# Performance work log

Hardware: AMD Instinct MI355X
Metric: run time of the kernel (lower is better)

The kernel has to match this reference:

```python
import jax, jax.numpy as jnp
import numpy as np

B, NFIELD = 8192, 20
NFEAT = 100000
SQL_VOCAB = NFIELD + NFEAT + 1  # 100021
SQL_NEMB, DATA_NEMB = 16, 64
HID = 1024
OUT = 1
K = 16
ALPHA = 1.5
N_BISECT = 50


def entmax_bisect(x, alpha=ALPHA, n_iter=N_BISECT):
    # alpha-entmax via bisection on the threshold tau (Peters et al. 2019).
    am1 = alpha - 1.0
    x = x * am1
    d = x.shape[-1]
    max_val = jnp.max(x, axis=-1, keepdims=True)
    tau_lo = max_val - 1.0
    tau_hi = max_val - d ** (1.0 - alpha)

    def p(tau):
        return jnp.clip(x - tau, 0.0) ** (1.0 / am1)

    f_lo = jnp.sum(p(tau_lo), axis=-1, keepdims=True) - 1.0

    def body(carry, _):
        tau_lo, tau_hi, f_lo = carry
        tau_m = 0.5 * (tau_lo + tau_hi)
        f_m = jnp.sum(p(tau_m), axis=-1, keepdims=True) - 1.0
        same_side = (f_m * f_lo) >= 0
        tau_lo = jnp.where(same_side, tau_m, tau_lo)
        tau_hi = jnp.where(same_side, tau_hi, tau_m)
        f_lo = jnp.where(same_side, f_m, f_lo)
        return (tau_lo, tau_hi, f_lo), None

    (tau_lo, tau_hi, _), _ = jax.lax.scan(body, (tau_lo, tau_hi, f_lo), None, length=n_iter)
    pm = p(0.5 * (tau_lo + tau_hi))
    return pm / jnp.sum(pm, axis=-1, keepdims=True)


def cv_squared(v):
    eps = 1e-10
    var = jnp.var(v, ddof=1)  # torch .var() is unbiased
    mean = jnp.mean(v)
    return var / (mean * mean + eps)


def setup_inputs() -> dict:
    key = jax.random.key(0)
    ks = jax.random.split(key, 12)
    xavier = lambda k, shp: jax.random.uniform(k, shp, jnp.float32, -1.0, 1.0) * jnp.sqrt(6.0 / (shp[-2] + shp[-1]))
    inp = {
        "x": jax.random.randint(ks[0], (B, NFIELD), 0, NFEAT),
        "sql": jax.random.randint(ks[1], (B, NFIELD), 0, SQL_VOCAB),
        "sql_emb_table": xavier(ks[2], (SQL_VOCAB, SQL_NEMB)),
        "input_emb_table": xavier(ks[3], (NFEAT, DATA_NEMB)),
        # gate: Linear(gate_in, HID) -> ReLU -> Linear(HID, K)
        "gW1": xavier(ks[4], (NFIELD * SQL_NEMB, HID)),
        "gb1": jnp.zeros((HID,), jnp.float32),
        "gW2": xavier(ks[5], (HID, K)),
        "gb2": jnp.zeros((K,), jnp.float32),
        # K experts: Linear(in, HID) -> ReLU -> Linear(HID, OUT), stacked on axis 0
        "eW1": xavier(ks[6], (K, NFIELD * DATA_NEMB, HID)),
        "eb1": jnp.zeros((K, HID), jnp.float32),
        "eW2": xavier(ks[7], (K, HID, OUT)),
        "eb2": jnp.zeros((K, OUT), jnp.float32),
    }
    return inp


def reference(x, sql, sql_emb_table, input_emb_table, gW1, gb1, gW2, gb2, eW1, eb1, eW2, eb2):
    Bn = x.shape[0]
    x_emb = input_emb_table[x].reshape(Bn, -1)      # [B, nfield*data_nemb]
    sql_emb = sql_emb_table[sql].reshape(Bn, -1)    # [B, nfield*sql_nemb]

    # gate network + entmax-bisect (dropout is identity in eval)
    g = jax.nn.relu(sql_emb @ gW1 + gb1) @ gW2 + gb2  # [B, K]
    gate_score = entmax_bisect(g)                     # [B, K], sparse simplex

    loss = cv_squared(jnp.sum(gate_score, axis=0))

    # all K experts on every token, vectorized
    h = jax.nn.relu(jnp.einsum("bi,kih->bkh", x_emb, eW1) + eb1)  # [B, K, HID]
    y_k = jnp.einsum("bkh,kho->bko", h, eW2) + eb2                # [B, K, OUT]
    y = jnp.sum(gate_score[:, :, None] * y_k, axis=1)             # [B, OUT]
    return (y.squeeze(-1), loss)
```

## Files before the change

### kernel.cpp

```cpp
#include <hip/hip_runtime.h>
#include <stdint.h>

#define NFIELD 20
#define HID 1024
#define KEXP 16
#define KX 1280
#define KS 320
#define BATCH 8192

typedef __bf16 bf16x8 __attribute__((ext_vector_type(8)));
typedef float f32x4 __attribute__((ext_vector_type(4)));

__device__ __forceinline__ unsigned short f2bf(float f) {
  union { float f; unsigned u; } v; v.f = f;
  unsigned r = v.u + 0x7FFFu + ((v.u >> 16) & 1u);
  return (unsigned short)(r >> 16);
}

__device__ __forceinline__ void gload16(const void* g, void* l) {
  __builtin_amdgcn_global_load_lds(
      (const __attribute__((address_space(1))) unsigned int*)(uintptr_t)g,
      (__attribute__((address_space(3))) unsigned int*)(unsigned)(uintptr_t)l,
      16, 0, 0);
}


__global__ void transpose_cvt(const float* __restrict__ src, unsigned short* __restrict__ dst,
                              int R, int C, long sstride, long dstride) {
  __shared__ float tile[32][33];
  const float* s = src + (size_t)blockIdx.z * sstride;
  unsigned short* d = dst + (size_t)blockIdx.z * dstride;
  const int r0 = blockIdx.y * 32, c0 = blockIdx.x * 32;
  const int tx = threadIdx.x & 31, ty = threadIdx.x >> 5;
#pragma unroll
  for (int i = 0; i < 4; ++i)
    tile[ty + 8 * i][tx] = s[(size_t)(r0 + ty + 8 * i) * C + c0 + tx];
  __syncthreads();
#pragma unroll
  for (int i = 0; i < 4; ++i)
    d[(size_t)(c0 + ty + 8 * i) * R + r0 + tx] = f2bf(tile[tx][ty + 8 * i]);
}

__global__ void gather_x_k(const int* __restrict__ x, const float* __restrict__ tab,
                           unsigned short* __restrict__ out) {
  const int b = blockIdx.x;
  const int f = threadIdx.x >> 4;
  const int q = threadIdx.x & 15;
  const int idx = x[b * NFIELD + f];
  const float4 v = *(const float4*)(tab + (size_t)idx * 64 + q * 4);
  ushort4 o;
  o.x = f2bf(v.x); o.y = f2bf(v.y); o.z = f2bf(v.z); o.w = f2bf(v.w);
  *(ushort4*)(out + (size_t)b * KX + f * 64 + q * 4) = o;
}

__global__ void gather_sql_k(const int* __restrict__ sql, const float* __restrict__ tab,
                             unsigned short* __restrict__ out) {
  const int t = blockIdx.x * 256 + threadIdx.x;
  const int b = t / 80;
  const int r = t - b * 80;
  const int f = r >> 2, q = r & 3;
  const int idx = sql[b * NFIELD + f];
  const float4 v = *(const float4*)(tab + (size_t)idx * 16 + q * 4);
  ushort4 o;
  o.x = f2bf(v.x); o.y = f2bf(v.y); o.z = f2bf(v.z); o.w = f2bf(v.w);
  *(ushort4*)(out + (size_t)b * KS + f * 16 + q * 4) = o;
}

template <int NJO, int KTOT>
__global__ __launch_bounds__(256) void gemm_fused(const __bf16* __restrict__ A,
                                                  const __bf16* __restrict__ Bt,
                                                  const float* __restrict__ bias,
                                                  const float* __restrict__ W2,
                                                  float* __restrict__ out) {
  alignas(16) __shared__ __bf16 As[128][64];
  alignas(16) __shared__ __bf16 Bs[128][64];
  const int tid = threadIdx.x;
  const int lane = tid & 63;
  const int wave = tid >> 6;
  const int wr = wave >> 1, wc = wave & 1;
  const int m0 = blockIdx.y * 128;
  const int n0 = blockIdx.x * 128;
  const int srow = lane >> 3;
  const int schunk = (lane & 7) ^ srow;
  const int r15 = lane & 15, g4 = lane >> 4;

  f32x4 acc[4][4] = {};

  for (int kt = 0; kt < KTOT / 64; ++kt) {
#pragma unroll
    for (int i = 0; i < 4; ++i) {
      const int rb = wave * 32 + i * 8;
      gload16(A + (size_t)(m0 + rb + srow) * KTOT + kt * 64 + schunk * 8, (void*)&As[rb][0]);
    }
#pragma unroll
    for (int i = 0; i < 4; ++i) {
      const int rb = wave * 32 + i * 8;
      gload16(Bt + (size_t)(n0 + rb + srow) * KTOT + kt * 64 + schunk * 8, (void*)&Bs[rb][0]);
    }
    __syncthreads();
#pragma unroll
    for (int kk = 0; kk < 2; ++kk) {
      bf16x8 af[4], bfr[4];
      const int c = kk * 4 + g4;
#pragma unroll
      for (int mi = 0; mi < 4; ++mi) {
        const int row = wr * 64 + mi * 16 + r15;
        af[mi] = *(const bf16x8*)&As[row][(c ^ (row & 7)) * 8];
      }
#pragma unroll
      for (int ni = 0; ni < 4; ++ni) {
        const int row = wc * 64 + ni * 16 + r15;
        bfr[ni] = *(const bf16x8*)&Bs[row][(c ^ (row & 7)) * 8];
      }
#pragma unroll
      for (int mi = 0; mi < 4; ++mi)
#pragma unroll
        for (int ni = 0; ni < 4; ++ni)
          acc[mi][ni] = __builtin_amdgcn_mfma_f32_16x16x32_bf16(af[mi], bfr[ni], acc[mi][ni], 0, 0, 0);
    }
    __syncthreads();
  }

  int ncol[4];
  float bsv[4];
#pragma unroll
  for (int ni = 0; ni < 4; ++ni) {
    ncol[ni] = n0 + wc * 64 + ni * 16 + r15;
    bsv[ni] = bias[ncol[ni]];
  }
#pragma unroll
  for (int mi = 0; mi < 4; ++mi)
#pragma unroll
    for (int ni = 0; ni < 4; ++ni)
#pragma unroll
      for (int j = 0; j < 4; ++j) {
        float v = acc[mi][ni][j] + bsv[ni];
        acc[mi][ni][j] = v > 0.f ? v : 0.f;
      }
#pragma unroll
  for (int jo = 0; jo < NJO; ++jo) {
    float w4[4];
#pragma unroll
    for (int ni = 0; ni < 4; ++ni)
      w4[ni] = (NJO == 1) ? W2[ncol[ni]] : W2[ncol[ni] * NJO + jo];
#pragma unroll
    for (int mi = 0; mi < 4; ++mi)
#pragma unroll
      for (int j = 0; j < 4; ++j) {
        float s = acc[mi][0][j] * w4[0] + acc[mi][1][j] * w4[1] +
                  acc[mi][2][j] * w4[2] + acc[mi][3][j] * w4[3];
        s += __shfl_xor(s, 1);
        s += __shfl_xor(s, 2);
        s += __shfl_xor(s, 4);
        s += __shfl_xor(s, 8);
        if (r15 == 0) {
          const int row = m0 + wr * 64 + mi * 16 + g4 * 4 + j;
          const int oc = (NJO == 1) ? (n0 >> 10) : jo;
          atomicAdd(&out[row * KEXP + oc], s);
        }
      }
  }
}

__global__ void entmax_combine(const float* __restrict__ gacc, const float* __restrict__ gb2,
                               const float* __restrict__ yk, const float* __restrict__ eb2,
                               float* __restrict__ y, double* __restrict__ colsum) {
  const int b = blockIdx.x * 256 + threadIdx.x;
  float x[16];
  float mx = -3.4e38f;
#pragma unroll
  for (int j = 0; j < 16; ++j) {
    x[j] = (gacc[b * 16 + j] + gb2[j]) * 0.5f;
    mx = fmaxf(mx, x[j]);
  }
  float lo = mx - 1.0f, hi = mx - 0.25f;
  float flo = -1.0f;
#pragma unroll
  for (int j = 0; j < 16; ++j) {
    float d = x[j] - lo; d = d > 0.f ? d : 0.f;
    flo += d * d;
  }
  for (int it = 0; it < 50; ++it) {
    const float tm = 0.5f * (lo + hi);
    float fm = -1.0f;
#pragma unroll
    for (int j = 0; j < 16; ++j) {
      float d = x[j] - tm; d = d > 0.f ? d : 0.f;
      fm += d * d;
    }
    if (fm * flo >= 0.f) { lo = tm; flo = fm; } else { hi = tm; }
  }
  const float tm = 0.5f * (lo + hi);
  float p[16], ps = 0.f;
#pragma unroll
  for (int j = 0; j < 16; ++j) {
    float d = x[j] - tm; d = d > 0.f ? d : 0.f;
    p[j] = d * d; ps += p[j];
  }
  const float inv = 1.0f / ps;
  float yv = 0.f;
#pragma unroll
  for (int j = 0; j < 16; ++j) {
    p[j] *= inv;
    yv += p[j] * (yk[b * 16 + j] + eb2[j]);
  }
  y[b] = yv;

  const int lane = threadIdx.x & 63, wv = threadIdx.x >> 6;
  __shared__ float red[4][16];
#pragma unroll
  for (int j = 0; j < 16; ++j) {
    float v = p[j];
    v += __shfl_xor(v, 1);  v += __shfl_xor(v, 2);  v += __shfl_xor(v, 4);
    v += __shfl_xor(v, 8);  v += __shfl_xor(v, 16); v += __shfl_xor(v, 32);
    if (lane == 0) red[wv][j] = v;
  }
  __syncthreads();
  if (threadIdx.x < 16) {
    double s = (double)red[0][threadIdx.x] + (double)red[1][threadIdx.x] +
               (double)red[2][threadIdx.x] + (double)red[3][threadIdx.x];
    atomicAdd(&colsum[threadIdx.x], s);
  }
}

__global__ void loss_k(const double* __restrict__ colsum, float* __restrict__ out) {
  if (threadIdx.x == 0 && blockIdx.x == 0) {
    double m = 0.0;
    for (int k = 0; k < 16; ++k) m += colsum[k];
    m *= (1.0 / 16.0);
    double var = 0.0;
    for (int k = 0; k < 16; ++k) { const double d = colsum[k] - m; var += d * d; }
    var *= (1.0 / 15.0);
    out[0] = (float)(var / (m * m + 1e-10));
  }
}

extern "C" void kernel_launch(void* const* d_in, const int* in_sizes, int n_in,
                              void* d_out, int out_size, void* d_ws, size_t ws_size,
                              hipStream_t stream) {
  const int*   x    = (const int*)d_in[0];
  const int*   sql  = (const int*)d_in[1];
  const float* sqlT = (const float*)d_in[2];
  const float* inT  = (const float*)d_in[3];
  const float* gW1  = (const float*)d_in[4];
  const float* gb1  = (const float*)d_in[5];
  const float* gW2  = (const float*)d_in[6];
  const float* gb2  = (const float*)d_in[7];
  const float* eW1  = (const float*)d_in[8];
  const float* eb1  = (const float*)d_in[9];
  const float* eW2  = (const float*)d_in[10];
  const float* eb2  = (const float*)d_in[11];

  char* ws = (char*)d_ws;
  unsigned short* eW1T = (unsigned short*)(ws);
  unsigned short* xemb = (unsigned short*)(ws + 41943040);
  unsigned short* semb = (unsigned short*)(ws + 62914560);
  unsigned short* gW1T = (unsigned short*)(ws + 68157440);
  float*  yk     = (float*)(ws + 68812800);
  float*  gacc   = (float*)(ws + 69337088);
  double* colsum = (double*)(ws + 69861376);

  hipMemsetAsync(yk, 0, 524288 * 2 + 128, stream);

  transpose_cvt<<<dim3(32, 40, 16), 256, 0, stream>>>(eW1, eW1T, 1280, 1024, 1280L * 1024, 1024L * 1280);
  transpose_cvt<<<dim3(32, 10, 1), 256, 0, stream>>>(gW1, gW1T, 320, 1024, 0, 0);
  gather_x_k<<<BATCH, 320, 0, stream>>>(x, inT, xemb);
  gather_sql_k<<<BATCH * 80 / 256, 256, 0, stream>>>(sql, sqlT, semb);

  gemm_fused<1, KX><<<dim3(16384 / 128, BATCH / 128), 256, 0, stream>>>(
      (const __bf16*)xemb, (const __bf16*)eW1T, eb1, eW2, yk);
  gemm_fused<16, KS><<<dim3(HID / 128, BATCH / 128), 256, 0, stream>>>(
      (const __bf16*)semb, (const __bf16*)gW1T, gb1, gW2, gacc);

  entmax_combine<<<BATCH / 256, 256, 0, stream>>>(gacc, gb2, yk, eb2, (float*)d_out, colsum);
  loss_k<<<1, 64, 0, stream>>>(colsum, (float*)d_out + BATCH);
}
```

Measured before the change: 627.9 us.

## Rewrite fused GEMM as 256x256 double-buffered pipelined kernel with XCD swizzle

Replaces the 128x128 single-buffered GEMM with a 256x256 tile kernel using 8 waves and double-buffered LDS, issuing next-tile global-to-LDS loads interleaved with MFMA phases. It uses raw s_barrier/vmcnt waits and s_setprio around the MFMA bursts, and remaps the workgroup index so neighbouring tiles land on the same XCD. The aim is to hide load latency, raise arithmetic intensity and improve L2 locality. In exchange it needs 128KB of LDS per block, more registers for the accumulators, and hand-counted waitcnt logic that is fragile. The gate GEMM gets only 128 blocks, which may underfill the device.

```diff
diff --git a/kernel.cpp b/kernel.cpp
--- a/kernel.cpp
+++ b/kernel.cpp
@@ -23,6 +23,8 @@
       (__attribute__((address_space(3))) unsigned int*)(unsigned)(uintptr_t)l,
       16, 0, 0);
 }
+
+#define SBAR() asm volatile("s_barrier" ::: "memory")
 
 
 __global__ void transpose_cvt(const float* __restrict__ src, unsigned short* __restrict__ dst,
@@ -67,58 +69,114 @@
 }
 
 template <int NJO, int KTOT>
-__global__ __launch_bounds__(256) void gemm_fused(const __bf16* __restrict__ A,
+__global__ __launch_bounds__(512, 2) void gemm256(const __bf16* __restrict__ A,
                                                   const __bf16* __restrict__ Bt,
                                                   const float* __restrict__ bias,
                                                   const float* __restrict__ W2,
                                                   float* __restrict__ out) {
-  alignas(16) __shared__ __bf16 As[128][64];
-  alignas(16) __shared__ __bf16 Bs[128][64];
+  constexpr int NT = KTOT / 64;
+  alignas(16) __shared__ __bf16 As[2][256][64];
+  alignas(16) __shared__ __bf16 Bs[2][256][64];
+
   const int tid = threadIdx.x;
   const int lane = tid & 63;
   const int wave = tid >> 6;
-  const int wr = wave >> 1, wc = wave & 1;
-  const int m0 = blockIdx.y * 128;
-  const int n0 = blockIdx.x * 128;
+  const int wr = wave >> 2;
+  const int wc = wave & 3;
+
+  unsigned flat = blockIdx.y * gridDim.x + blockIdx.x;
+  const unsigned nwg = gridDim.x * gridDim.y;
+  flat = (flat & 7u) * (nwg >> 3) + (flat >> 3);
+  const int m0 = (int)(flat / gridDim.x) * 256;
+  const int n0 = (int)(flat % gridDim.x) * 256;
+
   const int srow = lane >> 3;
   const int schunk = (lane & 7) ^ srow;
   const int r15 = lane & 15, g4 = lane >> 4;
 
-  f32x4 acc[4][4] = {};
-
-  for (int kt = 0; kt < KTOT / 64; ++kt) {
-#pragma unroll
-    for (int i = 0; i < 4; ++i) {
-      const int rb = wave * 32 + i * 8;
-      gload16(A + (size_t)(m0 + rb + srow) * KTOT + kt * 64 + schunk * 8, (void*)&As[rb][0]);
+  const __bf16* Ag = A + (size_t)(m0 + srow) * KTOT + schunk * 8;
+  const __bf16* Bg = Bt + (size_t)(n0 + srow) * KTOT + schunk * 8;
+
+  auto stageA = [&](int t, int h) {
+    const int c = t & 1;
+#pragma unroll
+    for (int i = 0; i < 2; ++i) {
+      const int rb = h * 128 + (wave + 8 * i) * 8;
+      gload16(Ag + (size_t)rb * KTOT + t * 64, (void*)&As[c][rb][0]);
     }
-#pragma unroll
-    for (int i = 0; i < 4; ++i) {
-      const int rb = wave * 32 + i * 8;
-      gload16(Bt + (size_t)(n0 + rb + srow) * KTOT + kt * 64 + schunk * 8, (void*)&Bs[rb][0]);
+  };
+  auto stageB = [&](int t, int h) {
+    const int c = t & 1;
+#pragma unroll
+    for (int i = 0; i < 2; ++i) {
+      const int rb = h * 128 + (wave + 8 * i) * 8;
+      gload16(Bg + (size_t)rb * KTOT + t * 64, (void*)&Bs[c][rb][0]);
     }
-    __syncthreads();
-#pragma unroll
-    for (int kk = 0; kk < 2; ++kk) {
-      bf16x8 af[4], bfr[4];
-      const int c = kk * 4 + g4;
-#pragma unroll
-      for (int mi = 0; mi < 4; ++mi) {
-        const int row = wr * 64 + mi * 16 + r15;
-        af[mi] = *(const bf16x8*)&As[row][(c ^ (row & 7)) * 8];
+  };
+  auto rdA = [&](int c, int mi, int kk) -> bf16x8 {
+    const int row = wr * 128 + mi * 16 + r15;
+    const int ch = (kk * 4 + g4) ^ (row & 7);
+    return *(const bf16x8*)&As[c][row][ch * 8];
+  };
+  auto rdB = [&](int c, int ni, int kk) -> bf16x8 {
+    const int row = wc * 64 + ni * 16 + r15;
+    const int ch = (kk * 4 + g4) ^ (row & 7);
+    return *(const bf16x8*)&Bs[c][row][ch * 8];
+  };
+
+  f32x4 acc[8][4] = {};
+
+  stageA(0, 0); stageA(0, 1);
+  stageB(0, 0); stageB(0, 1);
+  if (NT > 1) {
+    stageB(1, 0); stageB(1, 1);
+    asm volatile("s_waitcnt vmcnt(4)" ::: "memory");
+  } else {
+    asm volatile("s_waitcnt vmcnt(0)" ::: "memory");
+  }
+  SBAR();
+
+#pragma unroll 2
+  for (int t = 0; t < NT; ++t) {
+    const int c = t & 1;
+    bf16x8 bfr[4][2];
+#pragma unroll
+    for (int q = 0; q < 4; ++q) {
+      if (q == 0) {
+#pragma unroll
+        for (int ni = 0; ni < 4; ++ni) {
+          bfr[ni][0] = rdB(c, ni, 0);
+          bfr[ni][1] = rdB(c, ni, 1);
+        }
       }
-#pragma unroll
-      for (int ni = 0; ni < 4; ++ni) {
-        const int row = wc * 64 + ni * 16 + r15;
-        bfr[ni] = *(const bf16x8*)&Bs[row][(c ^ (row & 7)) * 8];
+      bf16x8 af[2][2];
+#pragma unroll
+      for (int d = 0; d < 2; ++d)
+#pragma unroll
+        for (int kk = 0; kk < 2; ++kk) af[d][kk] = rdA(c, q * 2 + d, kk);
+
+      if (q == 0 && t + 1 < NT) stageA(t + 1, 0);
+      if (q == 1 && t + 1 < NT) stageA(t + 1, 1);
+      if (q == 2 && t + 2 < NT) stageB(t + 2, 0);
+      if (q == 3 && t + 2 < NT) stageB(t + 2, 1);
+
+      SBAR();
+      __builtin_amdgcn_s_setprio(1);
+#pragma unroll
+      for (int d = 0; d < 2; ++d)
+#pragma unroll
+        for (int ni = 0; ni < 4; ++ni)
+#pragma unroll
+          for (int kk = 0; kk < 2; ++kk)
+            acc[q * 2 + d][ni] = __builtin_amdgcn_mfma_f32_16x16x32_bf16(
+                af[d][kk], bfr[ni][kk], acc[q * 2 + d][ni], 0, 0, 0);
+      __builtin_amdgcn_s_setprio(0);
+      if (q == 3) {
+        if (t < NT - 2) asm volatile("s_waitcnt vmcnt(4)" ::: "memory");
+        else            asm volatile("s_waitcnt vmcnt(0)" ::: "memory");
       }
-#pragma unroll
-      for (int mi = 0; mi < 4; ++mi)
-#pragma unroll
-        for (int ni = 0; ni < 4; ++ni)
-          acc[mi][ni] = __builtin_amdgcn_mfma_f32_16x16x32_bf16(af[mi], bfr[ni], acc[mi][ni], 0, 0, 0);
+      SBAR();
     }
-    __syncthreads();
   }
 
   int ncol[4];
@@ -129,7 +187,7 @@
     bsv[ni] = bias[ncol[ni]];
   }
 #pragma unroll
-  for (int mi = 0; mi < 4; ++mi)
+  for (int mi = 0; mi < 8; ++mi)
 #pragma unroll
     for (int ni = 0; ni < 4; ++ni)
 #pragma unroll
@@ -144,7 +202,7 @@
     for (int ni = 0; ni < 4; ++ni)
       w4[ni] = (NJO == 1) ? W2[ncol[ni]] : W2[ncol[ni] * NJO + jo];
 #pragma unroll
-    for (int mi = 0; mi < 4; ++mi)
+    for (int mi = 0; mi < 8; ++mi)
 #pragma unroll
       for (int j = 0; j < 4; ++j) {
         float s = acc[mi][0][j] * w4[0] + acc[mi][1][j] * w4[1] +
@@ -154,7 +212,7 @@
         s += __shfl_xor(s, 4);
         s += __shfl_xor(s, 8);
         if (r15 == 0) {
-          const int row = m0 + wr * 64 + mi * 16 + g4 * 4 + j;
+          const int row = m0 + wr * 128 + mi * 16 + g4 * 4 + j;
           const int oc = (NJO == 1) ? (n0 >> 10) : jo;
           atomicAdd(&out[row * KEXP + oc], s);
         }
@@ -267,9 +325,9 @@
   gather_x_k<<<BATCH, 320, 0, stream>>>(x, inT, xemb);
   gather_sql_k<<<BATCH * 80 / 256, 256, 0, stream>>>(sql, sqlT, semb);
 
-  gemm_fused<1, KX><<<dim3(16384 / 128, BATCH / 128), 256, 0, stream>>>(
+  gemm256<1, KX><<<dim3(16384 / 256, BATCH / 256), 512, 0, stream>>>(
       (const __bf16*)xemb, (const __bf16*)eW1T, eb1, eW2, yk);
-  gemm_fused<16, KS><<<dim3(HID / 128, BATCH / 128), 256, 0, stream>>>(
+  gemm256<16, KS><<<dim3(HID / 256, BATCH / 256), 512, 0, stream>>>(
       (const __bf16*)semb, (const __bf16*)gW1T, gb1, gW2, gacc);
 
   entmax_combine<<<BATCH / 256, 256, 0, stream>>>(gacc, gb2, yk, eb2, (float*)d_out, colsum);
```

After: 594.3 us. -5.3%, faster.

## Double-buffer GEMM LDS tiles with 512-thread 128x256 blocks and XCD-aware block remap

Applied to the files above, without the earlier changes.

The fused expert/gate GEMM is restructured so each block uses 8 waves on a 128x256 tile with a BK of 32. LDS is double-buffered so global_load_lds prefetch of tile t+2 overlaps the MFMAs, with s_waitcnt/s_barrier and setprio interleaving. Block IDs are remapped across the 8 XCDs to improve L2 locality. The goal is to hide global-load latency and raise MFMA utilisation. In exchange the synchronisation is more intricate, and the epilogue, not shown, must still match the new 256-column tile and 4-column-wave layout.

```diff
diff --git a/kernel.cpp b/kernel.cpp
--- a/kernel.cpp
+++ b/kernel.cpp
@@ -23,6 +23,8 @@
       (__attribute__((address_space(3))) unsigned int*)(unsigned)(uintptr_t)l,
       16, 0, 0);
 }
+
+#define SBAR() asm volatile("s_barrier" ::: "memory")
 
 
 __global__ void transpose_cvt(const float* __restrict__ src, unsigned short* __restrict__ dst,
@@ -67,58 +69,83 @@
 }
 
 template <int NJO, int KTOT>
-__global__ __launch_bounds__(256) void gemm_fused(const __bf16* __restrict__ A,
-                                                  const __bf16* __restrict__ Bt,
-                                                  const float* __restrict__ bias,
-                                                  const float* __restrict__ W2,
-                                                  float* __restrict__ out) {
-  alignas(16) __shared__ __bf16 As[128][64];
-  alignas(16) __shared__ __bf16 Bs[128][64];
+__global__ __launch_bounds__(512, 4) void gemm_k(const __bf16* __restrict__ A,
+                                                 const __bf16* __restrict__ Bt,
+                                                 const float* __restrict__ bias,
+                                                 const float* __restrict__ W2,
+                                                 float* __restrict__ out) {
+  constexpr int NT = KTOT / 32;
+  alignas(16) __shared__ __bf16 As[2][128][32];
+  alignas(16) __shared__ __bf16 Bs[2][256][32];
+
   const int tid = threadIdx.x;
   const int lane = tid & 63;
   const int wave = tid >> 6;
-  const int wr = wave >> 1, wc = wave & 1;
-  const int m0 = blockIdx.y * 128;
-  const int n0 = blockIdx.x * 128;
-  const int srow = lane >> 3;
-  const int schunk = (lane & 7) ^ srow;
+  const int wr = wave >> 2;
+  const int wc = wave & 3;
+
+  unsigned flat = blockIdx.y * gridDim.x + blockIdx.x;
+  const unsigned nwg = gridDim.x * gridDim.y;
+  flat = (flat & 7u) * (nwg >> 3) + (flat >> 3);
+  const int m0 = (int)(flat / gridDim.x) * 128;
+  const int n0 = (int)(flat % gridDim.x) * 256;
+
+  const int srow = lane >> 2;
+  const int sch = (lane & 3) ^ (srow & 3);
   const int r15 = lane & 15, g4 = lane >> 4;
 
+  const __bf16* Ag  = A  + (size_t)(m0 + wave * 16 + srow) * KTOT + sch * 8;
+  const __bf16* Bg0 = Bt + (size_t)(n0 + wave * 32 + srow) * KTOT + sch * 8;
+  const __bf16* Bg1 = Bt + (size_t)(n0 + wave * 32 + 16 + srow) * KTOT + sch * 8;
+
+  auto stage = [&](int t) {
+    const int c = t & 1;
+    gload16(Ag  + (size_t)t * 32, (void*)&As[c][wave * 16][0]);
+    gload16(Bg0 + (size_t)t * 32, (void*)&Bs[c][wave * 32][0]);
+    gload16(Bg1 + (size_t)t * 32, (void*)&Bs[c][wave * 32 + 16][0]);
+  };
+
   f32x4 acc[4][4] = {};
 
-  for (int kt = 0; kt < KTOT / 64; ++kt) {
-#pragma unroll
-    for (int i = 0; i < 4; ++i) {
-      const int rb = wave * 32 + i * 8;
-      gload16(A + (size_t)(m0 + rb + srow) * KTOT + kt * 64 + schunk * 8, (void*)&As[rb][0]);
+  stage(0);
+  if (NT > 1) { stage(1); asm volatile("s_waitcnt vmcnt(3)" ::: "memory"); }
+  else        {           asm volatile("s_waitcnt vmcnt(0)" ::: "memory"); }
+  SBAR();
+
+#pragma unroll 2
+  for (int t = 0; t < NT; ++t) {
+    const int c = t & 1;
+    bf16x8 af[4], bfr[4];
+#pragma unroll
+    for (int mi = 0; mi < 4; ++mi) {
+      const int row = wr * 64 + mi * 16 + r15;
+      af[mi] = *(const bf16x8*)&As[c][row][(g4 ^ (row & 3)) * 8];
     }
 #pragma unroll
-    for (int i = 0; i < 4; ++i) {
-      const int rb = wave * 32 + i * 8;
-      gload16(Bt + (size_t)(n0 + rb + srow) * KTOT + kt * 64 + schunk * 8, (void*)&Bs[rb][0]);
+    for (int ni = 0; ni < 4; ++ni) {
+      const int row = wc * 64 + ni * 16 + r15;
+      bfr[ni] = *(const bf16x8*)&Bs[c][row][(g4 ^ (row & 3)) * 8];
     }
-    __syncthreads();
-#pragma unroll
-    for (int kk = 0; kk < 2; ++kk) {
-      bf16x8 af[4], bfr[4];
-      const int c = kk * 4 + g4;
-#pragma unroll
-      for (int mi = 0; mi < 4; ++mi) {
-        const int row = wr * 64 + mi * 16 + r15;
-        af[mi] = *(const bf16x8*)&As[row][(c ^ (row & 7)) * 8];
-      }
-#pragma unroll
-      for (int ni = 0; ni < 4; ++ni) {
-        const int row = wc * 64 + ni * 16 + r15;
-        bfr[ni] = *(const bf16x8*)&Bs[row][(c ^ (row & 7)) * 8];
-      }
-#pragma unroll
-      for (int mi = 0; mi < 4; ++mi)
-#pragma unroll
-        for (int ni = 0; ni < 4; ++ni)
-          acc[mi][ni] = __builtin_amdgcn_mfma_f32_16x16x32_bf16(af[mi], bfr[ni], acc[mi][ni], 0, 0, 0);
-    }
-    __syncthreads();
+    SBAR();
+    __builtin_amdgcn_s_setprio(1);
+#pragma unroll
+    for (int mi = 0; mi < 2; ++mi)
+#pragma unroll
+      for (int ni = 0; ni < 4; ++ni)
+        acc[mi][ni] = __builtin_amdgcn_mfma_f32_16x16x32_bf16(af[mi], bfr[ni], acc[mi][ni], 0, 0, 0);
+    __builtin_amdgcn_s_setprio(0);
+    SBAR();
+    if (t + 2 < NT) stage(t + 2);
+    __builtin_amdgcn_s_setprio(1);
+#pragma unroll
+    for (int mi = 2; mi < 4; ++mi)
+#pragma unroll
+      for (int ni = 0; ni < 4; ++ni)
+        acc[mi][ni] = __builtin_amdgcn_mfma_f32_16x16x32_bf16(af[mi], bfr[ni], acc[mi][ni], 0, 0, 0);
+    __builtin_amdgcn_s_setprio(0);
+    if (t + 2 < NT) asm volatile("s_waitcnt vmcnt(3)" ::: "memory");
+    else            asm volatile("s_waitcnt vmcnt(0)" ::: "memory");
+    SBAR();
   }
 
   int ncol[4];
@@ -267,9 +294,9 @@
   gather_x_k<<<BATCH, 320, 0, stream>>>(x, inT, xemb);
   gather_sql_k<<<BATCH * 80 / 256, 256, 0, stream>>>(sql, sqlT, semb);
 
-  gemm_fused<1, KX><<<dim3(16384 / 128, BATCH / 128), 256, 0, stream>>>(
+  gemm_k<1, KX><<<dim3(16384 / 256, BATCH / 128), 512, 0, stream>>>(
       (const __bf16*)xemb, (const __bf16*)eW1T, eb1, eW2, yk);
-  gemm_fused<16, KS><<<dim3(HID / 128, BATCH / 128), 256, 0, stream>>>(
+  gemm_k<16, KS><<<dim3(HID / 256, BATCH / 128), 512, 0, stream>>>(
       (const __bf16*)semb, (const __bf16*)gW1T, gb1, gW2, gacc);
 
   entmax_combine<<<BATCH / 256, 256, 0, stream>>>(gacc, gb2, yk, eb2, (float*)d_out, colsum);
```

Result: slower. 664.6 us (+5.8%).
